# Optimization experiments

Measured on AMD Instinct MI355X. Metric: run time of the kernel, lower is better.

Reference implementation:

```python
import jax, jax.numpy as jnp
import numpy as np

N_NODES = 50000
N_EDGES = 800000
IN_CH = 128
HID = 64
HEADS = 4
OUT_CH = 10
NUM_GRAPHS = 500
NEG_SLOPE = 0.2  # PyG GATConv default LeakyReLU slope


def gat_conv(x, src, dst, W, a_src, a_dst, b, concat):
    """One PyG-style GATConv (inference; attention dropout disabled).
    x: [N, F_in], src/dst: [E'] (self-loops already appended).
    W: [F_in, H*C], a_src/a_dst: [H, C], b: [H*C] or [C].
    """
    N = x.shape[0]
    H, C = a_src.shape
    h = (x @ W).reshape(N, H, C)                      # [N,H,C]
    al_s = jnp.einsum('nhc,hc->nh', h, a_src)          # [N,H]
    al_d = jnp.einsum('nhc,hc->nh', h, a_dst)          # [N,H]
    e = al_s[src] + al_d[dst]                          # [E,H]
    e = jnp.where(e > 0, e, NEG_SLOPE * e)             # leaky_relu
    # segment softmax over edges sharing the same destination node
    e_max = jax.ops.segment_max(e, dst, num_segments=N)
    ex = jnp.exp(e - e_max[dst])
    denom = jax.ops.segment_sum(ex, dst, num_segments=N)
    alpha = ex / (denom[dst] + 1e-16)                  # [E,H]
    msg = h[src] * alpha[:, :, None]                   # [E,H,C]
    out = jax.ops.segment_sum(msg, dst, num_segments=N)  # [N,H,C]
    out = out.reshape(N, H * C) if concat else out.mean(axis=1)
    return out + b


def _forward(x, edge_index, batch, W1, a_src1, a_dst1, b1,
             W2, a_src2, a_dst2, b2, fc_w, fc_b):
    N = x.shape[0]
    loops = jnp.arange(N, dtype=edge_index.dtype)
    src = jnp.concatenate([edge_index[0], loops])
    dst = jnp.concatenate([edge_index[1], loops])
    h = gat_conv(x, src, dst, W1, a_src1, a_dst1, b1, concat=True)
    h = jax.nn.relu(h)                                  # dropout: eval mode
    h = gat_conv(h, src, dst, W2, a_src2, a_dst2, b2, concat=False)
    pooled = jax.ops.segment_sum(h, batch, num_segments=NUM_GRAPHS)  # global_add_pool
    logits = pooled @ fc_w + fc_b
    return jax.nn.log_softmax(logits, axis=1)


def setup_inputs() -> dict:
    key = jax.random.key(0)
    ks = jax.random.split(key, 12)
    g = lambda k, shp, fan: jax.random.normal(k, shp, dtype=jnp.float32) * (1.0 / np.sqrt(fan))
    x = jax.random.normal(ks[0], (N_NODES, IN_CH), dtype=jnp.float32)
    edge_index = jax.random.randint(ks[1], (2, N_EDGES), 0, N_NODES, dtype=jnp.int64)
    batch = jnp.sort(jax.random.randint(ks[2], (N_NODES,), 0, NUM_GRAPHS, dtype=jnp.int64))
    return {
        'x': x,
        'edge_index': edge_index,
        'batch': batch,
        'W1': g(ks[3], (IN_CH, HEADS * HID), IN_CH),
        'a_src1': g(ks[4], (HEADS, HID), HID),
        'a_dst1': g(ks[5], (HEADS, HID), HID),
        'b1': jnp.zeros((HEADS * HID,), dtype=jnp.float32),
        'W2': g(ks[6], (HEADS * HID, HID), HEADS * HID),
        'a_src2': g(ks[7], (1, HID), HID),
        'a_dst2': g(ks[8], (1, HID), HID),
        'b2': jnp.zeros((HID,), dtype=jnp.float32),
        'fc_w': g(ks[9], (HID, OUT_CH), HID),
        'fc_b': jnp.zeros((OUT_CH,), dtype=jnp.float32),
    }


def reference(x, edge_index, batch, W1, a_src1, a_dst1, b1,
              W2, a_src2, a_dst2, b2, fc_w, fc_b):
    return _forward(x, edge_index, batch, W1, a_src1, a_dst1, b1,
                    W2, a_src2, a_dst2, b2, fc_w, fc_b)
```

## Files before the change

kernel.cpp:

```cpp
#include <hip/hip_runtime.h>
#include <hip/hip_bf16.h>
#include <math.h>

#define N_NODES   50000
#define N_EDGES   800000
#define EP        (N_EDGES + N_NODES)
#define IN_CH     128
#define HID       64
#define HEADS     4
#define F1        (HEADS * HID)
#define OUT_CH    10
#define NUM_GRAPHS 500
#define NEG_SLOPE 0.2f
#define RPAD      132
#define NTILES    (N_NODES / 16)
#define SCAT_B    ((EP + 255) / 256)
#define CAP       64

typedef __attribute__((ext_vector_type(8))) short short8;
typedef __attribute__((ext_vector_type(4))) float floatx4;

__device__ __forceinline__ unsigned short f2bf(float f) {
    unsigned int u = __float_as_uint(f);
    u += 0x7FFFu + ((u >> 16) & 1u);
    return (unsigned short)(u >> 16);
}
__device__ __forceinline__ unsigned int pack_bf2(float lo, float hi) {
    return (unsigned int)f2bf(lo) | ((unsigned int)f2bf(hi) << 16);
}
__device__ __forceinline__ float bf_lo(unsigned int u) { return __uint_as_float(u << 16); }
__device__ __forceinline__ float bf_hi(unsigned int u) { return __uint_as_float(u & 0xFFFF0000u); }
__device__ __forceinline__ float bf1(unsigned short h) { return __uint_as_float(((unsigned int)h) << 16); }

__global__ void init_kernel(int* __restrict__ cnt,
                            const float* __restrict__ W1, unsigned short* __restrict__ W1p,
                            const float* __restrict__ W2, unsigned short* __restrict__ W2p)
{
    const int gid = blockIdx.x * blockDim.x + threadIdx.x;
    if (gid < N_NODES) cnt[gid] = 0;
    if (gid < 4096) {
        const int t = gid >> 8, kt = (gid >> 6) & 3, l = gid & 63;
        const int col = t * 16 + (l & 15);
        unsigned short* o = W1p + (size_t)((t * 4 + kt) * 64 + l) * 8;
        #pragma unroll
        for (int j = 0; j < 8; ++j) {
            const int k = kt * 32 + (l >> 4) * 8 + j;
            o[j] = f2bf(W1[k * F1 + col]);
        }
    } else if (gid < 6144) {
        const int g2 = gid - 4096;
        const int t = g2 >> 9, kt = (g2 >> 6) & 7, l = g2 & 63;
        const int col = t * 16 + (l & 15);
        unsigned short* o = W2p + (size_t)((t * 8 + kt) * 64 + l) * 8;
        #pragma unroll
        for (int j = 0; j < 8; ++j) {
            const int k = kt * 32 + (l >> 4) * 8 + j;
            o[j] = f2bf(W2[k * HID + col]);
        }
    }
}

__global__ __launch_bounds__(256) void scatter_gemm1(
    const int* __restrict__ ei, int* __restrict__ cnt,
    unsigned short* __restrict__ csr,
    const float* __restrict__ x, const short* __restrict__ W1p,
    const float* __restrict__ a_src1, const float* __restrict__ a_dst1,
    unsigned short* __restrict__ H1b,
    float* __restrict__ al_s1, float* __restrict__ al_d1)
{
    const int e = blockIdx.x * 256 + threadIdx.x;
    if (e < EP) {
        int src, dst;
        if (e < N_EDGES) { src = ei[e]; dst = ei[N_EDGES + e]; }
        else             { src = dst = e - N_EDGES; }
        const int slot = atomicAdd(&cnt[dst], 1);
        if (slot < CAP) csr[dst * CAP + slot] = (unsigned short)src;
    }
    if (blockIdx.x >= NTILES) return;

    const int m0 = blockIdx.x * 16;
    const int w = threadIdx.x >> 6;
    const int l = threadIdx.x & 63;
    const int q = l >> 4, r = l & 15;
    floatx4 acc[4] = {};
    const float* arow = x + (size_t)(m0 + r) * IN_CH + q * 8;
    #pragma unroll
    for (int kt = 0; kt < 4; ++kt) {
        const float4 f0 = *(const float4*)(arow + kt * 32);
        const float4 f1 = *(const float4*)(arow + kt * 32 + 4);
        union { uint4 u; short8 s; } a;
        a.u = make_uint4(pack_bf2(f0.x, f0.y), pack_bf2(f0.z, f0.w),
                         pack_bf2(f1.x, f1.y), pack_bf2(f1.z, f1.w));
        #pragma unroll
        for (int t = 0; t < 4; ++t) {
            const int nt = w * 4 + t;
            const short8 b = *(const short8*)(W1p + (size_t)((nt * 4 + kt) * 64 + l) * 8);
            acc[t] = __builtin_amdgcn_mfma_f32_16x16x32_bf16(a.s, b, acc[t], 0, 0, 0);
        }
    }
    float ls[4] = {0.f, 0.f, 0.f, 0.f}, ld[4] = {0.f, 0.f, 0.f, 0.f};
    #pragma unroll
    for (int t = 0; t < 4; ++t) {
        const int col = (w * 4 + t) * 16 + r;
        const float as = a_src1[col], ad = a_dst1[col];
        #pragma unroll
        for (int reg = 0; reg < 4; ++reg) {
            H1b[(size_t)(m0 + q * 4 + reg) * F1 + col] = f2bf(acc[t][reg]);
            ls[reg] += acc[t][reg] * as;
            ld[reg] += acc[t][reg] * ad;
        }
    }
    #pragma unroll
    for (int reg = 0; reg < 4; ++reg) {
        #pragma unroll
        for (int off = 8; off > 0; off >>= 1) {
            ls[reg] += __shfl_down(ls[reg], off, 16);
            ld[reg] += __shfl_down(ld[reg], off, 16);
        }
    }
    if (r == 0) {
        #pragma unroll
        for (int reg = 0; reg < 4; ++reg) {
            const int n = m0 + q * 4 + reg;
            al_s1[n * HEADS + w] = ls[reg];
            al_d1[n * HEADS + w] = ld[reg];
        }
    }
}

__global__ __launch_bounds__(256) void agg1_gemm2(
    const int* __restrict__ cnt, const unsigned short* __restrict__ csr,
    const float* __restrict__ al_s1, const float* __restrict__ al_d1,
    const uint2* __restrict__ H1b2, const float* __restrict__ b1,
    const short* __restrict__ W2p,
    const float* __restrict__ a_src2, const float* __restrict__ a_dst2,
    unsigned short* __restrict__ H2b,
    float* __restrict__ al_s2, float* __restrict__ al_d2)
{
    const int m0 = blockIdx.x * 16;
    const int w = threadIdx.x >> 6;
    const int l = threadIdx.x & 63;
    __shared__ unsigned int rows[16][RPAD];

    const int h = l >> 4;
    for (int d = 0; d < 4; ++d) {
        const int dst = m0 + w * 4 + d;
        const int n = min(cnt[dst], CAP);
        const float4 ad = *(const float4*)(al_d1 + dst * 4);
        float a0 = 0.f, a1 = 0.f, a2 = 0.f, a3 = 0.f, den = 0.f;
        int s_reg = 0;
        float w0 = 0.f, w1 = 0.f, w2 = 0.f, w3 = 0.f;
        if (l < n) {
            s_reg = csr[dst * CAP + l];
            const float4 as = *(const float4*)(al_s1 + s_reg * 4);
            float t0 = as.x + ad.x; t0 = t0 > 0.f ? t0 : NEG_SLOPE * t0;
            float t1 = as.y + ad.y; t1 = t1 > 0.f ? t1 : NEG_SLOPE * t1;
            float t2 = as.z + ad.z; t2 = t2 > 0.f ? t2 : NEG_SLOPE * t2;
            float t3 = as.w + ad.w; t3 = t3 > 0.f ? t3 : NEG_SLOPE * t3;
            w0 = __expf(t0); w1 = __expf(t1); w2 = __expf(t2); w3 = __expf(t3);
        }
        const int n4 = (n + 3) & ~3;
        for (int i = 0; i < n4; i += 4) {
            int   srcj[4];
            float wtj[4];
            #pragma unroll
            for (int j = 0; j < 4; ++j) {
                const int idx = i + j;
                srcj[j] = __shfl(s_reg, idx, 64);
                const float t0 = __shfl(w0, idx, 64);
                const float t1 = __shfl(w1, idx, 64);
                const float t2 = __shfl(w2, idx, 64);
                const float t3 = __shfl(w3, idx, 64);
                wtj[j] = h == 0 ? t0 : (h == 1 ? t1 : (h == 2 ? t2 : t3));
            }
            uint2 u[4];
            #pragma unroll
            for (int j = 0; j < 4; ++j)
                u[j] = H1b2[(size_t)srcj[j] * (F1 / 4) + l];
            #pragma unroll
            for (int j = 0; j < 4; ++j) {
                a0 += wtj[j] * bf_lo(u[j].x); a1 += wtj[j] * bf_hi(u[j].x);
                a2 += wtj[j] * bf_lo(u[j].y); a3 += wtj[j] * bf_hi(u[j].y);
                den += wtj[j];
            }
        }
        const float rcp = 1.f / (den + 1e-16f);
        const float4 bb = *(const float4*)(b1 + 4 * l);
        float v0 = a0 * rcp + bb.x; v0 = v0 > 0.f ? v0 : 0.f;
        float v1 = a1 * rcp + bb.y; v1 = v1 > 0.f ? v1 : 0.f;
        float v2 = a2 * rcp + bb.z; v2 = v2 > 0.f ? v2 : 0.f;
        float v3 = a3 * rcp + bb.w; v3 = v3 > 0.f ? v3 : 0.f;
        rows[w * 4 + d][2 * l]     = pack_bf2(v0, v1);
        rows[w * 4 + d][2 * l + 1] = pack_bf2(v2, v3);
    }
    __syncthreads();

    const int q = l >> 4, r = l & 15;
    floatx4 acc = {};
    #pragma unroll
    for (int kt = 0; kt < 8; ++kt) {
        union { uint4 u; short8 s; } a;
        a.u = *(const uint4*)&rows[r][kt * 16 + q * 4];
        const short8 b = *(const short8*)(W2p + (size_t)((w * 8 + kt) * 64 + l) * 8);
        acc = __builtin_amdgcn_mfma_f32_16x16x32_bf16(a.s, b, acc, 0, 0, 0);
    }
    const int col = w * 16 + r;
    const float as = a_src2[col], ad2 = a_dst2[col];
    float ls[4], ld[4];
    #pragma unroll
    for (int reg = 0; reg < 4; ++reg) {
        H2b[(size_t)(m0 + q * 4 + reg) * HID + col] = f2bf(acc[reg]);
        ls[reg] = acc[reg] * as;
        ld[reg] = acc[reg] * ad2;
    }
    #pragma unroll
    for (int reg = 0; reg < 4; ++reg) {
        #pragma unroll
        for (int off = 8; off > 0; off >>= 1) {
            ls[reg] += __shfl_down(ls[reg], off, 16);
            ld[reg] += __shfl_down(ld[reg], off, 16);
        }
    }
    __shared__ float Ls[4][16], Ld[4][16];
    if (r == 0) {
        #pragma unroll
        for (int reg = 0; reg < 4; ++reg) {
            Ls[w][q * 4 + reg] = ls[reg];
            Ld[w][q * 4 + reg] = ld[reg];
        }
    }
    __syncthreads();
    if (threadIdx.x < 16) {
        const int row = threadIdx.x;
        al_s2[m0 + row] = Ls[0][row] + Ls[1][row] + Ls[2][row] + Ls[3][row];
        al_d2[m0 + row] = Ld[0][row] + Ld[1][row] + Ld[2][row] + Ld[3][row];
    }
}

__global__ __launch_bounds__(256) void agg2_csr(
    const int* __restrict__ cnt, const unsigned short* __restrict__ csr,
    const float* __restrict__ al_s2, const float* __restrict__ al_d2,
    const uint2* __restrict__ H2b2, uint2* __restrict__ out2b)
{
    const int dst = blockIdx.x * 4 + (threadIdx.x >> 6);
    const int l = threadIdx.x & 63;
    const int qt = l >> 4, j = l & 15;
    const int n = min(cnt[dst], CAP);
    const float ad = al_d2[dst];
    float a0 = 0.f, a1 = 0.f, a2 = 0.f, a3 = 0.f, den = 0.f;
    int s_reg = 0;
    float w_reg = 0.f;
    if (l < n) {
        s_reg = csr[dst * CAP + l];
        float t = al_s2[s_reg] + ad;
        t = t > 0.f ? t : NEG_SLOPE * t;
        w_reg = __expf(t);
    }
    const int n8 = (n + 7) & ~7;
    for (int i = 0; i < n8; i += 8) {
        const int e0 = i + qt, e1 = i + 4 + qt;
        const int   src0 = __shfl(s_reg, e0, 64), src1 = __shfl(s_reg, e1, 64);
        const float wt0  = __shfl(w_reg, e0, 64), wt1  = __shfl(w_reg, e1, 64);
        const uint2 u0 = H2b2[(size_t)src0 * (HID / 4) + j];
        const uint2 u1 = H2b2[(size_t)src1 * (HID / 4) + j];
        a0 += wt0 * bf_lo(u0.x) + wt1 * bf_lo(u1.x);
        a1 += wt0 * bf_hi(u0.x) + wt1 * bf_hi(u1.x);
        a2 += wt0 * bf_lo(u0.y) + wt1 * bf_lo(u1.y);
        a3 += wt0 * bf_hi(u0.y) + wt1 * bf_hi(u1.y);
        den += wt0 + wt1;
    }
    #pragma unroll
    for (int m = 16; m <= 32; m <<= 1) {
        a0 += __shfl_xor(a0, m, 64);
        a1 += __shfl_xor(a1, m, 64);
        a2 += __shfl_xor(a2, m, 64);
        a3 += __shfl_xor(a3, m, 64);
        den += __shfl_xor(den, m, 64);
    }
    if (l < 16) {
        const float rcp = 1.f / (den + 1e-16f);
        out2b[(size_t)dst * (HID / 4) + j] =
            make_uint2(pack_bf2(a0 * rcp, a1 * rcp), pack_bf2(a2 * rcp, a3 * rcp));
    }
}

__global__ __launch_bounds__(256) void pool_fc_kernel(
    const unsigned short* __restrict__ out2b, const float* __restrict__ b2,
    const int* __restrict__ batch,
    const float* __restrict__ fc_w, const float* __restrict__ fc_b,
    float* __restrict__ out)
{
    const int g = blockIdx.x;
    const int q = threadIdx.x >> 6, c = threadIdx.x & 63;
    __shared__ int se[2];
    __shared__ float partial[4][HID];
    __shared__ float pl[HID];
    __shared__ float logits[OUT_CH];
    if (threadIdx.x < 2) {
        const int target = g + threadIdx.x;
        int lo = 0, hi = N_NODES;
        while (lo < hi) { int mid = (lo + hi) >> 1; if (batch[mid] < target) lo = mid + 1; else hi = mid; }
        se[threadIdx.x] = lo;
    }
    __syncthreads();
    const int start = se[0], end = se[1];
    float acc = 0.f;
    for (int n = start + q; n < end; n += 4)
        acc += bf1(out2b[(size_t)n * HID + c]);
    partial[q][c] = acc;
    __syncthreads();
    if (q == 0)
        pl[c] = partial[0][c] + partial[1][c] + partial[2][c] + partial[3][c]
              + (float)(end - start) * b2[c];
    __syncthreads();
    if (threadIdx.x < OUT_CH) {
        float l = fc_b[threadIdx.x];
        #pragma unroll
        for (int k = 0; k < HID; ++k) l += pl[k] * fc_w[k * OUT_CH + threadIdx.x];
        logits[threadIdx.x] = l;
    }
    __syncthreads();
    if (threadIdx.x == 0) {
        float m = logits[0];
        #pragma unroll
        for (int j2 = 1; j2 < OUT_CH; ++j2) m = fmaxf(m, logits[j2]);
        float s = 0.f;
        #pragma unroll
        for (int j2 = 0; j2 < OUT_CH; ++j2) s += __expf(logits[j2] - m);
        const float lse = m + __logf(s);
        #pragma unroll
        for (int j2 = 0; j2 < OUT_CH; ++j2) out[g * OUT_CH + j2] = logits[j2] - lse;
    }
}


extern "C" void kernel_launch(void* const* d_in, const int* in_sizes, int n_in,
                              void* d_out, int out_size, void* d_ws, size_t ws_size,
                              hipStream_t stream)
{
    const float* x      = (const float*)d_in[0];
    const int*   ei     = (const int*)  d_in[1];
    const int*   batch  = (const int*)  d_in[2];
    const float* W1     = (const float*)d_in[3];
    const float* a_src1 = (const float*)d_in[4];
    const float* a_dst1 = (const float*)d_in[5];
    const float* b1     = (const float*)d_in[6];
    const float* W2     = (const float*)d_in[7];
    const float* a_src2 = (const float*)d_in[8];
    const float* a_dst2 = (const float*)d_in[9];
    const float* b2     = (const float*)d_in[10];
    const float* fc_w   = (const float*)d_in[11];
    const float* fc_b   = (const float*)d_in[12];
    float* out = (float*)d_out;

    char* ws = (char*)d_ws;
    size_t off = 0;
    auto alloc_b = [&](size_t bytes) { void* p = (void*)(ws + off); off += (bytes + 15) & ~15ull; return p; };

    unsigned short* H1b  = (unsigned short*)alloc_b((size_t)N_NODES * F1 * 2);
    float* al_s1  = (float*)alloc_b((size_t)N_NODES * HEADS * 4);
    float* al_d1  = (float*)alloc_b((size_t)N_NODES * HEADS * 4);
    unsigned short* H2b  = (unsigned short*)alloc_b((size_t)N_NODES * HID * 2);
    float* al_s2  = (float*)alloc_b((size_t)N_NODES * 4);
    float* al_d2  = (float*)alloc_b((size_t)N_NODES * 4);
    unsigned short* out2b = (unsigned short*)alloc_b((size_t)N_NODES * HID * 2);
    int*   cnt    = (int*)alloc_b((size_t)N_NODES * 4);
    unsigned short* csr = (unsigned short*)alloc_b((size_t)N_NODES * CAP * 2);
    unsigned short* W1p = (unsigned short*)alloc_b((size_t)IN_CH * F1 * 2);
    unsigned short* W2p = (unsigned short*)alloc_b((size_t)F1 * HID * 2);

    init_kernel<<<(N_NODES + 255) / 256, 256, 0, stream>>>(cnt, W1, W1p, W2, W2p);

    scatter_gemm1<<<SCAT_B, 256, 0, stream>>>(ei, cnt, csr, x, (const short*)W1p,
                                              a_src1, a_dst1, H1b, al_s1, al_d1);

    agg1_gemm2<<<N_NODES / 16, 256, 0, stream>>>(cnt, csr, al_s1, al_d1,
                                                 (const uint2*)H1b, b1,
                                                 (const short*)W2p, a_src2, a_dst2,
                                                 H2b, al_s2, al_d2);

    agg2_csr<<<N_NODES / 4, 256, 0, stream>>>(cnt, csr, al_s2, al_d2,
                                              (const uint2*)H2b, (uint2*)out2b);

    pool_fc_kernel<<<NUM_GRAPHS, 256, 0, stream>>>(out2b, b2, batch, fc_w, fc_b, out);
}
```

Measured before the change: 248.6 us.

## Split padded CSR into hot/overflow halves, add nontemporal loads, unroll agg2

The per-destination padded adjacency buffer is split into a 32-slot primary array and a separate overflow array, so the commonly used slots (about 17 per node on average) sit in a denser region with less wasted footprint. Edge-index and feature reads plus H1 stores in the scatter/GEMM kernel become nontemporal to reduce cache pollution. The layer-2 aggregation loop gathers four neighbor rows per iteration instead of two, giving more loads in flight. This adds a branch on slot index when reading the adjacency, and rounds the loop up to 16 edges, which means more idle work for low-degree nodes.

```diff
diff --git a/kernel.cpp b/kernel.cpp
--- a/kernel.cpp
+++ b/kernel.cpp
@@ -15,10 +15,12 @@
 #define RPAD      132
 #define NTILES    (N_NODES / 16)
 #define SCAT_B    ((EP + 255) / 256)
-#define CAP       64
+#define CAPP      32
+#define CAPT      64
 
 typedef __attribute__((ext_vector_type(8))) short short8;
 typedef __attribute__((ext_vector_type(4))) float floatx4;
+typedef __attribute__((ext_vector_type(4))) float fv4;
 
 __device__ __forceinline__ unsigned short f2bf(float f) {
     unsigned int u = __float_as_uint(f);
@@ -62,7 +64,7 @@
 
 __global__ __launch_bounds__(256) void scatter_gemm1(
     const int* __restrict__ ei, int* __restrict__ cnt,
-    unsigned short* __restrict__ csr,
+    unsigned short* __restrict__ csrA, unsigned short* __restrict__ csrB,
     const float* __restrict__ x, const short* __restrict__ W1p,
     const float* __restrict__ a_src1, const float* __restrict__ a_dst1,
     unsigned short* __restrict__ H1b,
@@ -71,10 +73,15 @@
     const int e = blockIdx.x * 256 + threadIdx.x;
     if (e < EP) {
         int src, dst;
-        if (e < N_EDGES) { src = ei[e]; dst = ei[N_EDGES + e]; }
-        else             { src = dst = e - N_EDGES; }
+        if (e < N_EDGES) {
+            src = __builtin_nontemporal_load(ei + e);
+            dst = __builtin_nontemporal_load(ei + N_EDGES + e);
+        } else {
+            src = dst = e - N_EDGES;
+        }
         const int slot = atomicAdd(&cnt[dst], 1);
-        if (slot < CAP) csr[dst * CAP + slot] = (unsigned short)src;
+        if (slot < CAPP)      csrA[dst * CAPP + slot] = (unsigned short)src;
+        else if (slot < CAPT) csrB[dst * CAPP + (slot - CAPP)] = (unsigned short)src;
     }
     if (blockIdx.x >= NTILES) return;
 
@@ -86,8 +93,8 @@
     const float* arow = x + (size_t)(m0 + r) * IN_CH + q * 8;
     #pragma unroll
     for (int kt = 0; kt < 4; ++kt) {
-        const float4 f0 = *(const float4*)(arow + kt * 32);
-        const float4 f1 = *(const float4*)(arow + kt * 32 + 4);
+        const fv4 f0 = __builtin_nontemporal_load((const fv4*)(arow + kt * 32));
+        const fv4 f1 = __builtin_nontemporal_load((const fv4*)(arow + kt * 32 + 4));
         union { uint4 u; short8 s; } a;
         a.u = make_uint4(pack_bf2(f0.x, f0.y), pack_bf2(f0.z, f0.w),
                          pack_bf2(f1.x, f1.y), pack_bf2(f1.z, f1.w));
@@ -105,7 +112,8 @@
         const float as = a_src1[col], ad = a_dst1[col];
         #pragma unroll
         for (int reg = 0; reg < 4; ++reg) {
-            H1b[(size_t)(m0 + q * 4 + reg) * F1 + col] = f2bf(acc[t][reg]);
+            __builtin_nontemporal_store(f2bf(acc[t][reg]),
+                                        H1b + (size_t)(m0 + q * 4 + reg) * F1 + col);
             ls[reg] += acc[t][reg] * as;
             ld[reg] += acc[t][reg] * ad;
         }
@@ -129,7 +137,8 @@
 }
 
 __global__ __launch_bounds__(256) void agg1_gemm2(
-    const int* __restrict__ cnt, const unsigned short* __restrict__ csr,
+    const int* __restrict__ cnt,
+    const unsigned short* __restrict__ csrA, const unsigned short* __restrict__ csrB,
     const float* __restrict__ al_s1, const float* __restrict__ al_d1,
     const uint2* __restrict__ H1b2, const float* __restrict__ b1,
     const short* __restrict__ W2p,
@@ -145,13 +154,13 @@
     const int h = l >> 4;
     for (int d = 0; d < 4; ++d) {
         const int dst = m0 + w * 4 + d;
-        const int n = min(cnt[dst], CAP);
+        const int n = min(cnt[dst], CAPT);
         const float4 ad = *(const float4*)(al_d1 + dst * 4);
         float a0 = 0.f, a1 = 0.f, a2 = 0.f, a3 = 0.f, den = 0.f;
         int s_reg = 0;
         float w0 = 0.f, w1 = 0.f, w2 = 0.f, w3 = 0.f;
         if (l < n) {
-            s_reg = csr[dst * CAP + l];
+            s_reg = (l < CAPP) ? csrA[dst * CAPP + l] : csrB[dst * CAPP + (l - CAPP)];
             const float4 as = *(const float4*)(al_s1 + s_reg * 4);
             float t0 = as.x + ad.x; t0 = t0 > 0.f ? t0 : NEG_SLOPE * t0;
             float t1 = as.y + ad.y; t1 = t1 > 0.f ? t1 : NEG_SLOPE * t1;
@@ -238,36 +247,47 @@
 }
 
 __global__ __launch_bounds__(256) void agg2_csr(
-    const int* __restrict__ cnt, const unsigned short* __restrict__ csr,
+    const int* __restrict__ cnt,
+    const unsigned short* __restrict__ csrA, const unsigned short* __restrict__ csrB,
     const float* __restrict__ al_s2, const float* __restrict__ al_d2,
     const uint2* __restrict__ H2b2, uint2* __restrict__ out2b)
 {
     const int dst = blockIdx.x * 4 + (threadIdx.x >> 6);
     const int l = threadIdx.x & 63;
     const int qt = l >> 4, j = l & 15;
-    const int n = min(cnt[dst], CAP);
+    const int n = min(cnt[dst], CAPT);
     const float ad = al_d2[dst];
     float a0 = 0.f, a1 = 0.f, a2 = 0.f, a3 = 0.f, den = 0.f;
     int s_reg = 0;
     float w_reg = 0.f;
     if (l < n) {
-        s_reg = csr[dst * CAP + l];
+        s_reg = (l < CAPP) ? csrA[dst * CAPP + l] : csrB[dst * CAPP + (l - CAPP)];
         float t = al_s2[s_reg] + ad;
         t = t > 0.f ? t : NEG_SLOPE * t;
         w_reg = __expf(t);
     }
-    const int n8 = (n + 7) & ~7;
-    for (int i = 0; i < n8; i += 8) {
-        const int e0 = i + qt, e1 = i + 4 + qt;
-        const int   src0 = __shfl(s_reg, e0, 64), src1 = __shfl(s_reg, e1, 64);
-        const float wt0  = __shfl(w_reg, e0, 64), wt1  = __shfl(w_reg, e1, 64);
-        const uint2 u0 = H2b2[(size_t)src0 * (HID / 4) + j];
-        const uint2 u1 = H2b2[(size_t)src1 * (HID / 4) + j];
-        a0 += wt0 * bf_lo(u0.x) + wt1 * bf_lo(u1.x);
-        a1 += wt0 * bf_hi(u0.x) + wt1 * bf_hi(u1.x);
-        a2 += wt0 * bf_lo(u0.y) + wt1 * bf_lo(u1.y);
-        a3 += wt0 * bf_hi(u0.y) + wt1 * bf_hi(u1.y);
-        den += wt0 + wt1;
+    const int n16 = (n + 15) & ~15;
+    for (int i = 0; i < n16; i += 16) {
+        int   srcj[4];
+        float wtj[4];
+        #pragma unroll
+        for (int jj = 0; jj < 4; ++jj) {
+            const int idx = i + jj * 4 + qt;
+            srcj[jj] = __shfl(s_reg, idx, 64);
+            wtj[jj]  = __shfl(w_reg, idx, 64);
+        }
+        uint2 u[4];
+        #pragma unroll
+        for (int jj = 0; jj < 4; ++jj)
+            u[jj] = H2b2[(size_t)srcj[jj] * (HID / 4) + j];
+        #pragma unroll
+        for (int jj = 0; jj < 4; ++jj) {
+            a0 += wtj[jj] * bf_lo(u[jj].x);
+            a1 += wtj[jj] * bf_hi(u[jj].x);
+            a2 += wtj[jj] * bf_lo(u[jj].y);
+            a3 += wtj[jj] * bf_hi(u[jj].y);
+            den += wtj[jj];
+        }
     }
     #pragma unroll
     for (int m = 16; m <= 32; m <<= 1) {
@@ -365,21 +385,22 @@
     float* al_d2  = (float*)alloc_b((size_t)N_NODES * 4);
     unsigned short* out2b = (unsigned short*)alloc_b((size_t)N_NODES * HID * 2);
     int*   cnt    = (int*)alloc_b((size_t)N_NODES * 4);
-    unsigned short* csr = (unsigned short*)alloc_b((size_t)N_NODES * CAP * 2);
+    unsigned short* csrA = (unsigned short*)alloc_b((size_t)N_NODES * CAPP * 2);
+    unsigned short* csrB = (unsigned short*)alloc_b((size_t)N_NODES * CAPP * 2);
     unsigned short* W1p = (unsigned short*)alloc_b((size_t)IN_CH * F1 * 2);
     unsigned short* W2p = (unsigned short*)alloc_b((size_t)F1 * HID * 2);
 
     init_kernel<<<(N_NODES + 255) / 256, 256, 0, stream>>>(cnt, W1, W1p, W2, W2p);
 
-    scatter_gemm1<<<SCAT_B, 256, 0, stream>>>(ei, cnt, csr, x, (const short*)W1p,
+    scatter_gemm1<<<SCAT_B, 256, 0, stream>>>(ei, cnt, csrA, csrB, x, (const short*)W1p,
                                               a_src1, a_dst1, H1b, al_s1, al_d1);
 
-    agg1_gemm2<<<N_NODES / 16, 256, 0, stream>>>(cnt, csr, al_s1, al_d1,
+    agg1_gemm2<<<N_NODES / 16, 256, 0, stream>>>(cnt, csrA, csrB, al_s1, al_d1,
                                                  (const uint2*)H1b, b1,
                                                  (const short*)W2p, a_src2, a_dst2,
                                                  H2b, al_s2, al_d2);
 
-    agg2_csr<<<N_NODES / 4, 256, 0, stream>>>(cnt, csr, al_s2, al_d2,
+    agg2_csr<<<N_NODES / 4, 256, 0, stream>>>(cnt, csrA, csrB, al_s2, al_d2,
                                               (const uint2*)H2b, (uint2*)out2b);
 
     pool_fc_kernel<<<NUM_GRAPHS, 256, 0, stream>>>(out2b, b2, batch, fc_w, fc_b, out);
```

After: 280.1 us. +12.7%, slower.
